# Optimization experiments

Measured on AMD Instinct MI355X. Metric: run time of the kernel, lower is better.

Reference implementation:

```python
import jax, jax.numpy as jnp
import numpy as np

DIM = 768
NUM_HEADS = 12
HEAD_DIM = DIM // NUM_HEADS
ORDER_H = 8
RENORM = True
B, N = 4, 1024


def setup_inputs() -> dict:
    key = jax.random.key(0)
    ks = jax.random.split(key, 8)
    return {
        "x": jax.random.normal(ks[0], (B, N, DIM), dtype=jnp.float32),
        "qkv_w": jax.random.normal(ks[1], (3 * DIM, DIM), dtype=jnp.float32) * (DIM ** -0.5),
        "qkv_b": jax.random.normal(ks[2], (3 * DIM,), dtype=jnp.float32) * 0.02,
        "proj_w": jax.random.normal(ks[3], (DIM, DIM), dtype=jnp.float32) * (DIM ** -0.5),
        "proj_b": jax.random.normal(ks[4], (DIM,), dtype=jnp.float32) * 0.02,
        "lamb": jax.random.normal(ks[5], (NUM_HEADS,), dtype=jnp.float32) * 0.1,
        "gamma": 1.0 + jax.random.normal(ks[6], (NUM_HEADS,), dtype=jnp.float32) * 0.1,
        "delta": jax.random.normal(ks[7], (NUM_HEADS,), dtype=jnp.float32) * 0.1,
    }


def reference(x, qkv_w, qkv_b, proj_w, proj_b, lamb, gamma, delta):
    Bx, Nx, C = x.shape
    scale = HEAD_DIM ** -0.5
    # qkv: [B,N,3C] -> [3,B,H,N,hd]
    qkv = (x @ qkv_w.T + qkv_b).reshape(Bx, Nx, 3, NUM_HEADS, HEAD_DIM)
    qkv = jnp.transpose(qkv, (2, 0, 3, 1, 4))
    q, k, v = qkv[0], qkv[1], qkv[2]
    attn = jax.nn.softmax(jnp.einsum("bhid,bhjd->bhij", q, k) * scale, axis=-1)
    I = jnp.eye(Nx, dtype=attn.dtype)
    # GFSA high-order term: (h-1)*(A - I)@A + A
    high = (ORDER_H - 1) * jnp.einsum("bhik,bhkj->bhij", attn - I, attn) + attn
    beta_ = lamb[None, :, None, None]
    gamma_ = gamma[None, :, None, None]
    delta_ = delta[None, :, None, None]
    attn = delta_ * I + gamma_ * attn + beta_ * high
    if RENORM:
        attn = jnp.maximum(attn, 0.0)
        attn = attn / (attn.sum(axis=-1, keepdims=True) + 1e-9)
    out = jnp.einsum("bhij,bhjd->bhid", attn, v)  # [B,H,N,hd]
    out = jnp.transpose(out, (0, 2, 1, 3)).reshape(Bx, Nx, C)
    return out @ proj_w.T + proj_b
```

## Files before the change

kernel.cpp:

```cpp
#include <hip/hip_runtime.h>
#include <hip/hip_bf16.h>

#define DIMC 768
#define NH 12
#define HD 64
#define BB 4
#define NN 1024
#define BHT 48
#define QKVC 2304

typedef unsigned short u16;
typedef __attribute__((ext_vector_type(4))) unsigned short u16x4;
typedef __attribute__((ext_vector_type(8))) unsigned short u16x8;
typedef __attribute__((ext_vector_type(8))) short s16x8;
typedef __attribute__((ext_vector_type(4))) float f32x4;

#define GLD16(g, l) __builtin_amdgcn_global_load_lds( \
    (__attribute__((address_space(1))) void*)(g),     \
    (__attribute__((address_space(3))) void*)(l), 16, 0, 0)

__device__ __forceinline__ u16 f2bf(float f) {
    unsigned u = __float_as_uint(f);
    return (u16)((u + 0x7FFF + ((u >> 16) & 1)) >> 16);
}
__device__ __forceinline__ float bf2f(u16 v) {
    return __uint_as_float(((unsigned)v) << 16);
}
struct bfp { u16 h, l; };
__device__ __forceinline__ bfp splitf(float f) {
    bfp r;
    r.h = f2bf(f);
    r.l = f2bf(f - bf2f(r.h));
    return r;
}

__device__ __forceinline__ int swz_linear() {
    const int nwg = gridDim.x * gridDim.y * gridDim.z;
    const int L = blockIdx.x + gridDim.x * (blockIdx.y + gridDim.y * blockIdx.z);
    return (L & 7) * (nwg >> 3) + (L >> 3);
}

__global__ __launch_bounds__(256) void split_f2b(
    const float* __restrict__ src, u16* __restrict__ hi, u16* __restrict__ lo,
    int n4)
{
    int idx = blockIdx.x * 256 + threadIdx.x;
    if (idx >= n4) return;
    float4 v = *(const float4*)&src[idx * 4];
    u16x4 h, l;
    bfp s;
    s = splitf(v.x); h[0] = s.h; l[0] = s.l;
    s = splitf(v.y); h[1] = s.h; l[1] = s.l;
    s = splitf(v.z); h[2] = s.h; l[2] = s.l;
    s = splitf(v.w); h[3] = s.h; l[3] = s.l;
    *(u16x4*)&hi[idx * 4] = h;
    *(u16x4*)&lo[idx * 4] = l;
}

__global__ __launch_bounds__(256, 3) void gemm3_mfma(
    int Mrows, int Nout, int K,
    const u16* __restrict__ Ahp, const u16* __restrict__ Alp,
    const u16* __restrict__ Bhp, const u16* __restrict__ Blp,
    const float* __restrict__ bias, float* __restrict__ C)
{
    __shared__ alignas(16) u16 sAh[128 * 32], sAl[128 * 32], sBh[128 * 32], sBl[128 * 32];
    const int tid = threadIdx.x;
    const int W = swz_linear();
    const int j0 = (W % gridDim.x) * 128, i0 = (W / gridDim.x) * 128;
    const int w = tid >> 6, l = tid & 63;
    const int wr = w >> 1, wc = w & 1;
    const int l15 = l & 15, kb4 = l >> 4;
    const int lrow = l >> 2, lch = (l & 3) * 8;

    f32x4 acc[4][4];
    const f32x4 zero = {0.f, 0.f, 0.f, 0.f};
#pragma unroll
    for (int a = 0; a < 4; ++a)
#pragma unroll
        for (int b = 0; b < 4; ++b) acc[a][b] = zero;

    for (int k0 = 0; k0 < K; k0 += 32) {
#pragma unroll
        for (int t = 0; t < 2; ++t) {
            const int r = w * 32 + t * 16;
            const size_t ar = (size_t)(i0 + r + lrow) * K + k0 + lch;
            const size_t br = (size_t)(j0 + r + lrow) * K + k0 + lch;
            GLD16(&Ahp[ar], &sAh[r * 32]);
            GLD16(&Alp[ar], &sAl[r * 32]);
            GLD16(&Bhp[br], &sBh[r * 32]);
            GLD16(&Blp[br], &sBl[r * 32]);
        }
        __syncthreads();

        s16x8 ah[4], al[4], bh[4], bl[4];
#pragma unroll
        for (int f = 0; f < 4; ++f) {
            const int ao = (wr * 64 + f * 16 + l15) * 32 + kb4 * 8;
            const int bo = (wc * 64 + f * 16 + l15) * 32 + kb4 * 8;
            ah[f] = *(const s16x8*)&sAh[ao];
            al[f] = *(const s16x8*)&sAl[ao];
            bh[f] = *(const s16x8*)&sBh[bo];
            bl[f] = *(const s16x8*)&sBl[bo];
        }
#pragma unroll
        for (int fr = 0; fr < 4; ++fr)
#pragma unroll
            for (int fc = 0; fc < 4; ++fc) {
                acc[fr][fc] = __builtin_amdgcn_mfma_f32_16x16x32_bf16(
                    ah[fr], bh[fc], acc[fr][fc], 0, 0, 0);
                acc[fr][fc] = __builtin_amdgcn_mfma_f32_16x16x32_bf16(
                    ah[fr], bl[fc], acc[fr][fc], 0, 0, 0);
                acc[fr][fc] = __builtin_amdgcn_mfma_f32_16x16x32_bf16(
                    al[fr], bh[fc], acc[fr][fc], 0, 0, 0);
            }
        __syncthreads();
    }

#pragma unroll
    for (int fr = 0; fr < 4; ++fr)
#pragma unroll
        for (int r = 0; r < 4; ++r) {
            const int gi = i0 + wr * 64 + fr * 16 + kb4 * 4 + r;
#pragma unroll
            for (int fc = 0; fc < 4; ++fc) {
                const int gj = j0 + wc * 64 + fc * 16 + l15;
                C[(size_t)gi * Nout + gj] = acc[fr][fc][r] + bias[gj];
            }
        }
}

__global__ __launch_bounds__(256, 3) void qkv_fused_mfma(
    const u16* __restrict__ Ahp, const u16* __restrict__ Alp,
    const u16* __restrict__ Bhp, const u16* __restrict__ Blp,
    const float* __restrict__ bias,
    u16* __restrict__ qh, u16* __restrict__ ql,
    u16* __restrict__ kh, u16* __restrict__ kl,
    u16* __restrict__ vth, u16* __restrict__ vtl)
{
    __shared__ alignas(16) u16 sAh[128 * 32], sAl[128 * 32], sBh[128 * 32], sBl[128 * 32];
    const int tid = threadIdx.x;
    const int W = swz_linear();
    const int j0 = (W % gridDim.x) * 128, i0 = (W / gridDim.x) * 128;
    const int w = tid >> 6, l = tid & 63;
    const int wr = w >> 1, wc = w & 1;
    const int l15 = l & 15, kb4 = l >> 4;
    const int lrow = l >> 2, lch = (l & 3) * 8;
    const int K = DIMC;

    f32x4 acc[4][4];
    const f32x4 zero = {0.f, 0.f, 0.f, 0.f};
#pragma unroll
    for (int a = 0; a < 4; ++a)
#pragma unroll
        for (int b = 0; b < 4; ++b) acc[a][b] = zero;

    for (int k0 = 0; k0 < K; k0 += 32) {
#pragma unroll
        for (int t = 0; t < 2; ++t) {
            const int r = w * 32 + t * 16;
            const size_t ar = (size_t)(i0 + r + lrow) * K + k0 + lch;
            const size_t br = (size_t)(j0 + r + lrow) * K + k0 + lch;
            GLD16(&Ahp[ar], &sAh[r * 32]);
            GLD16(&Alp[ar], &sAl[r * 32]);
            GLD16(&Bhp[br], &sBh[r * 32]);
            GLD16(&Blp[br], &sBl[r * 32]);
        }
        __syncthreads();

        s16x8 ah[4], al[4], bh[4], bl[4];
#pragma unroll
        for (int f = 0; f < 4; ++f) {
            const int ao = (wr * 64 + f * 16 + l15) * 32 + kb4 * 8;
            const int bo = (wc * 64 + f * 16 + l15) * 32 + kb4 * 8;
            ah[f] = *(const s16x8*)&sAh[ao];
            al[f] = *(const s16x8*)&sAl[ao];
            bh[f] = *(const s16x8*)&sBh[bo];
            bl[f] = *(const s16x8*)&sBl[bo];
        }
#pragma unroll
        for (int fr = 0; fr < 4; ++fr)
#pragma unroll
            for (int fc = 0; fc < 4; ++fc) {
                acc[fr][fc] = __builtin_amdgcn_mfma_f32_16x16x32_bf16(
                    ah[fr], bh[fc], acc[fr][fc], 0, 0, 0);
                acc[fr][fc] = __builtin_amdgcn_mfma_f32_16x16x32_bf16(
                    ah[fr], bl[fc], acc[fr][fc], 0, 0, 0);
                acc[fr][fc] = __builtin_amdgcn_mfma_f32_16x16x32_bf16(
                    al[fr], bh[fc], acc[fr][fc], 0, 0, 0);
            }
        __syncthreads();
    }

    const int part = j0 / DIMC;
    const int hbase = (j0 % DIMC) >> 6;
    const int h = hbase + wc;

#pragma unroll
    for (int fr = 0; fr < 4; ++fr) {
        const int rowbase = i0 + wr * 64 + fr * 16 + kb4 * 4;
        const int b = rowbase >> 10;
        const int n0 = rowbase & 1023;
        const int bh = b * NH + h;
#pragma unroll
        for (int fc = 0; fc < 4; ++fc) {
            const int gj = j0 + wc * 64 + fc * 16 + l15;
            const float bv = bias[gj];
            const int d = fc * 16 + l15;
            if (part == 0) {
#pragma unroll
                for (int r = 0; r < 4; ++r) {
                    bfp s = splitf((acc[fr][fc][r] + bv) * 0.125f);
                    const size_t o = ((size_t)bh * NN + n0 + r) * HD + d;
                    qh[o] = s.h; ql[o] = s.l;
                }
            } else if (part == 1) {
#pragma unroll
                for (int r = 0; r < 4; ++r) {
                    bfp s = splitf(acc[fr][fc][r] + bv);
                    const size_t o = ((size_t)bh * NN + n0 + r) * HD + d;
                    kh[o] = s.h; kl[o] = s.l;
                }
            } else {
                u16x4 hv, lv;
#pragma unroll
                for (int r = 0; r < 4; ++r) {
                    bfp s = splitf(acc[fr][fc][r] + bv);
                    hv[r] = s.h; lv[r] = s.l;
                }
                const size_t o = ((size_t)bh * HD + d) * NN + n0;
                *(u16x4*)&vth[o] = hv;
                *(u16x4*)&vtl[o] = lv;
            }
        }
    }
}

__global__ __launch_bounds__(256, 4) void qk_mfma(
    const u16* __restrict__ qh, const u16* __restrict__ ql,
    const u16* __restrict__ kh, const u16* __restrict__ kl,
    float* __restrict__ Sb, int h0)
{
    __shared__ alignas(16) u16 sAh[128 * 32], sAl[128 * 32], sBh[128 * 32], sBl[128 * 32];
    const int tid = threadIdx.x;
    const int W = swz_linear();
    const int bhl = W >> 6;
    const int ib = W & 63;
    const int j0 = (ib & 7) * 128, i0 = (ib >> 3) * 128;
    const int bh = h0 + bhl;
    const int w = tid >> 6, l = tid & 63;
    const int wr = w >> 1, wc = w & 1;
    const int l15 = l & 15, kb4 = l >> 4;
    const int lrow = l >> 2, lch = (l & 3) * 8;

    f32x4 acc[4][4];
    const f32x4 zero = {0.f, 0.f, 0.f, 0.f};
#pragma unroll
    for (int a = 0; a < 4; ++a)
#pragma unroll
        for (int b = 0; b < 4; ++b) acc[a][b] = zero;

    for (int k0 = 0; k0 < HD; k0 += 32) {
#pragma unroll
        for (int t = 0; t < 2; ++t) {
            const int r = w * 32 + t * 16;
            const size_t ar = ((size_t)bh * NN + i0 + r + lrow) * HD + k0 + lch;
            const size_t br = ((size_t)bh * NN + j0 + r + lrow) * HD + k0 + lch;
            GLD16(&qh[ar], &sAh[r * 32]);
            GLD16(&ql[ar], &sAl[r * 32]);
            GLD16(&kh[br], &sBh[r * 32]);
            GLD16(&kl[br], &sBl[r * 32]);
        }
        __syncthreads();

        s16x8 ah[4], al[4], bh[4], bl[4];
#pragma unroll
        for (int f = 0; f < 4; ++f) {
            const int ao = (wr * 64 + f * 16 + l15) * 32 + kb4 * 8;
            const int bo = (wc * 64 + f * 16 + l15) * 32 + kb4 * 8;
            ah[f] = *(const s16x8*)&sAh[ao];
            al[f] = *(const s16x8*)&sAl[ao];
            bh[f] = *(const s16x8*)&sBh[bo];
            bl[f] = *(const s16x8*)&sBl[bo];
        }
#pragma unroll
        for (int fr = 0; fr < 4; ++fr)
#pragma unroll
            for (int fc = 0; fc < 4; ++fc) {
                acc[fr][fc] = __builtin_amdgcn_mfma_f32_16x16x32_bf16(
                    ah[fr], bh[fc], acc[fr][fc], 0, 0, 0);
                acc[fr][fc] = __builtin_amdgcn_mfma_f32_16x16x32_bf16(
                    ah[fr], bl[fc], acc[fr][fc], 0, 0, 0);
                acc[fr][fc] = __builtin_amdgcn_mfma_f32_16x16x32_bf16(
                    al[fr], bh[fc], acc[fr][fc], 0, 0, 0);
            }
        __syncthreads();
    }

    float* Sh = Sb + (size_t)bhl * NN * NN;
#pragma unroll
    for (int fr = 0; fr < 4; ++fr)
#pragma unroll
        for (int r = 0; r < 4; ++r) {
            const int gi = i0 + wr * 64 + fr * 16 + kb4 * 4 + r;
#pragma unroll
            for (int fc = 0; fc < 4; ++fc) {
                const int gj = j0 + wc * 64 + fc * 16 + l15;
                Sh[(size_t)gi * NN + gj] = acc[fr][fc][r];
            }
        }
}

__global__ __launch_bounds__(256) void softmax_w(
    const float* __restrict__ Sb, u16* __restrict__ Abf)
{
    const int w = threadIdx.x >> 6, l = threadIdx.x & 63;
    const int row = blockIdx.x * 4 + w;
    const float* p = Sb + (size_t)row * NN;
    u16* q = Abf + (size_t)row * NN;

    float4 v[4];
    float m = -1e30f;
#pragma unroll
    for (int c = 0; c < 4; ++c) {
        v[c] = *(const float4*)&p[c * 256 + l * 4];
        m = fmaxf(m, fmaxf(fmaxf(v[c].x, v[c].y), fmaxf(v[c].z, v[c].w)));
    }
#pragma unroll
    for (int off = 32; off >= 1; off >>= 1) m = fmaxf(m, __shfl_xor(m, off));

    float s = 0.f;
#pragma unroll
    for (int c = 0; c < 4; ++c) {
        v[c].x = expf(v[c].x - m); v[c].y = expf(v[c].y - m);
        v[c].z = expf(v[c].z - m); v[c].w = expf(v[c].w - m);
        s += v[c].x + v[c].y + v[c].z + v[c].w;
    }
#pragma unroll
    for (int off = 32; off >= 1; off >>= 1) s += __shfl_xor(s, off);

    const float inv = 1.0f / s;
#pragma unroll
    for (int c = 0; c < 4; ++c) {
        u16x4 o;
        o[0] = f2bf(v[c].x * inv); o[1] = f2bf(v[c].y * inv);
        o[2] = f2bf(v[c].z * inv); o[3] = f2bf(v[c].w * inv);
        *(u16x4*)&q[c * 256 + l * 4] = o;
    }
}

__global__ __launch_bounds__(256, 4) void mpow_mfma(
    const u16* __restrict__ Abf, u16* __restrict__ Mb,
    const float* __restrict__ lamb, const float* __restrict__ gamma,
    const float* __restrict__ delta, int h0)
{
    __shared__ alignas(16) u16 sA[128 * 32], sB[128 * 32];
    const int tid = threadIdx.x;
    const int W = swz_linear();
    const int bz = W >> 6;
    const int ib = W & 63;
    const int j0 = (ib & 7) * 128, i0 = (ib >> 3) * 128;
    const int h = (h0 + bz) % NH;
    const u16* Ah = Abf + (size_t)bz * NN * NN;

    const int w = tid >> 6, l = tid & 63;
    const int wr = w >> 1, wc = w & 1;
    const int l15 = l & 15, kb4 = l >> 4;
    const int lrow = l >> 2;
    const int lchz = (((l & 3) ^ ((lrow >> 1) & 3)) * 8);
    const int swf = (l15 >> 1) & 3;
    const int kr = tid & 31;
    const int jc = (tid >> 5) * 16;
    const int krc = kr >> 3, kri = kr & 7;

    f32x4 acc[4][4];
    const f32x4 zero = {0.f, 0.f, 0.f, 0.f};
#pragma unroll
    for (int a = 0; a < 4; ++a)
#pragma unroll
        for (int b = 0; b < 4; ++b) acc[a][b] = zero;

    for (int k0 = 0; k0 < NN; k0 += 32) {
#pragma unroll
        for (int t = 0; t < 2; ++t) {
            const int r = w * 32 + t * 16;
            GLD16(&Ah[(size_t)(i0 + r + lrow) * NN + k0 + lchz], &sA[r * 32]);
        }
        {
            const u16* arow = &Ah[(size_t)(k0 + kr) * NN + j0 + jc];
            u16x8 b0 = *(const u16x8*)arow;
            u16x8 b1 = *(const u16x8*)(arow + 8);
#pragma unroll
            for (int e = 0; e < 8; ++e) {
                const int j1 = jc + e;
                const int j2 = jc + 8 + e;
                sB[j1 * 32 + ((krc ^ ((j1 >> 1) & 3)) * 8) + kri] = b0[e];
                sB[j2 * 32 + ((krc ^ ((j2 >> 1) & 3)) * 8) + kri] = b1[e];
            }
        }
        __syncthreads();

        s16x8 af[4], bf[4];
#pragma unroll
        for (int f = 0; f < 4; ++f) {
            const int co = (kb4 ^ swf) * 8;
            af[f] = *(const s16x8*)&sA[(wr * 64 + f * 16 + l15) * 32 + co];
            bf[f] = *(const s16x8*)&sB[(wc * 64 + f * 16 + l15) * 32 + co];
        }
#pragma unroll
        for (int fr = 0; fr < 4; ++fr)
#pragma unroll
            for (int fc = 0; fc < 4; ++fc)
                acc[fr][fc] = __builtin_amdgcn_mfma_f32_16x16x32_bf16(
                    af[fr], bf[fc], acc[fr][fc], 0, 0, 0);
        __syncthreads();
    }

    const float lam = lamb[h];
    const float c1 = gamma[h] - 6.0f * lam;
    const float c2 = 7.0f * lam;
    const float del = delta[h];
    u16* Mh = Mb + (size_t)bz * NN * NN;

#pragma unroll
    for (int fr = 0; fr < 4; ++fr)
#pragma unroll
        for (int r = 0; r < 4; ++r) {
            const int gi = i0 + wr * 64 + fr * 16 + kb4 * 4 + r;
#pragma unroll
            for (int fc = 0; fc < 4; ++fc) {
                const int gj = j0 + wc * 64 + fc * 16 + l15;
                const float a = bf2f(Ah[(size_t)gi * NN + gj]);
                float m = c2 * acc[fr][fc][r] + c1 * a + (gi == gj ? del : 0.f);
                m = fmaxf(m, 0.f);
                Mh[(size_t)gi * NN + gj] = f2bf(m);
            }
        }
}

__global__ __launch_bounds__(256, 4) void pv_mfma(
    const u16* __restrict__ Mb,
    const u16* __restrict__ vth, const u16* __restrict__ vtl,
    u16* __restrict__ aoh, u16* __restrict__ aol, int h0)
{
    __shared__ alignas(16) u16 sM[128 * 32], sVh[64 * 32], sVl[64 * 32];
    const int tid = threadIdx.x;
    const int W = swz_linear();
    const int bhl = W >> 3;
    const int i0 = (W & 7) * 128;
    const int bh = h0 + bhl;
    const int b = bh / NH, h = bh % NH;
    const u16* Mh = Mb + (size_t)bhl * NN * NN;
    const u16* vhb = vth + (size_t)bh * HD * NN;
    const u16* vlb = vtl + (size_t)bh * HD * NN;

    const int w = tid >> 6, l = tid & 63;
    const int l15 = l & 15, kb4 = l >> 4;
    const int lrow = l >> 2, lch = (l & 3) * 8;

    f32x4 acc[2][4], accs[2];
    const f32x4 zero = {0.f, 0.f, 0.f, 0.f};
#pragma unroll
    for (int a = 0; a < 2; ++a) {
#pragma unroll
        for (int c = 0; c < 4; ++c) acc[a][c] = zero;
        accs[a] = zero;
    }
    s16x8 ones;
#pragma unroll
    for (int e = 0; e < 8; ++e) ones[e] = (short)0x3F80;

    for (int k0 = 0; k0 < NN; k0 += 32) {
#pragma unroll
        for (int t = 0; t < 2; ++t) {
            const int r = w * 32 + t * 16;
            GLD16(&Mh[(size_t)(i0 + r + lrow) * NN + k0 + lch], &sM[r * 32]);
        }
        {
            const int r = w * 16;
            const size_t vr = (size_t)(r + lrow) * NN + k0 + lch;
            GLD16(&vhb[vr], &sVh[r * 32]);
            GLD16(&vlb[vr], &sVl[r * 32]);
        }
        __syncthreads();

        s16x8 af[2], bh[4], bl[4];
#pragma unroll
        for (int f = 0; f < 2; ++f)
            af[f] = *(const s16x8*)&sM[(w * 32 + f * 16 + l15) * 32 + kb4 * 8];
#pragma unroll
        for (int f = 0; f < 4; ++f) {
            bh[f] = *(const s16x8*)&sVh[(f * 16 + l15) * 32 + kb4 * 8];
            bl[f] = *(const s16x8*)&sVl[(f * 16 + l15) * 32 + kb4 * 8];
        }
#pragma unroll
        for (int fr = 0; fr < 2; ++fr) {
#pragma unroll
            for (int fc = 0; fc < 4; ++fc) {
                acc[fr][fc] = __builtin_amdgcn_mfma_f32_16x16x32_bf16(
                    af[fr], bh[fc], acc[fr][fc], 0, 0, 0);
                acc[fr][fc] = __builtin_amdgcn_mfma_f32_16x16x32_bf16(
                    af[fr], bl[fc], acc[fr][fc], 0, 0, 0);
            }
            accs[fr] = __builtin_amdgcn_mfma_f32_16x16x32_bf16(
                af[fr], ones, accs[fr], 0, 0, 0);
        }
        __syncthreads();
    }

#pragma unroll
    for (int fr = 0; fr < 2; ++fr)
#pragma unroll
        for (int r = 0; r < 4; ++r) {
            const int gi = i0 + w * 32 + fr * 16 + kb4 * 4 + r;
            const float inv = 1.0f / (accs[fr][r] + 1e-9f);
            const size_t ob = (size_t)(b * NN + gi) * DIMC + h * HD;
#pragma unroll
            for (int fc = 0; fc < 4; ++fc) {
                const int gd = fc * 16 + l15;
                bfp s = splitf(acc[fr][fc][r] * inv);
                aoh[ob + gd] = s.h;
                aol[ob + gd] = s.l;
            }
        }
}

extern "C" void kernel_launch(void* const* d_in, const int* in_sizes, int n_in,
                              void* d_out, int out_size, void* d_ws, size_t ws_size,
                              hipStream_t stream)
{
    const float* x      = (const float*)d_in[0];
    const float* qkv_w  = (const float*)d_in[1];
    const float* qkv_b  = (const float*)d_in[2];
    const float* proj_w = (const float*)d_in[3];
    const float* proj_b = (const float*)d_in[4];
    const float* lamb   = (const float*)d_in[5];
    const float* gamma  = (const float*)d_in[6];
    const float* delta  = (const float*)d_in[7];

    char* p = (char*)d_ws;
    u16* xh  = (u16*)p;                     p += (size_t)4096 * DIMC * 2;
    u16* xl  = (u16*)p;                     p += (size_t)4096 * DIMC * 2;
    u16* wh  = (u16*)p;                     p += (size_t)QKVC * DIMC * 2;
    u16* wl  = (u16*)p;                     p += (size_t)QKVC * DIMC * 2;
    u16* pwh = (u16*)p;                     p += (size_t)DIMC * DIMC * 2;
    u16* pwl = (u16*)p;                     p += (size_t)DIMC * DIMC * 2;
    u16* qh  = (u16*)p;                     p += (size_t)BHT * NN * HD * 2;
    u16* ql  = (u16*)p;                     p += (size_t)BHT * NN * HD * 2;
    u16* kh  = (u16*)p;                     p += (size_t)BHT * NN * HD * 2;
    u16* kl  = (u16*)p;                     p += (size_t)BHT * NN * HD * 2;
    u16* vth = (u16*)p;                     p += (size_t)BHT * HD * NN * 2;
    u16* vtl = (u16*)p;                     p += (size_t)BHT * HD * NN * 2;
    u16* aoh = (u16*)p;                     p += (size_t)4096 * DIMC * 2;
    u16* aol = (u16*)p;                     p += (size_t)4096 * DIMC * 2;
    const size_t fixed = (size_t)(p - (char*)d_ws);

    const size_t perh = (size_t)NN * NN * 4 + (size_t)NN * NN * 2;
    static const int choices[] = {48, 24, 16, 12, 8, 6, 4, 3, 2, 1};
    int CH = 1;
    for (int ci = 0; ci < 10; ++ci) {
        int c = choices[ci];
        if (fixed + (size_t)c * perh <= ws_size) { CH = c; break; }
    }

    float* Sb = (float*)p;                  p += (size_t)CH * NN * NN * 4;
    u16* Abf  = (u16*)p;                    p += (size_t)CH * NN * NN * 2;
    u16* Mb   = (u16*)Sb;

    split_f2b<<<dim3((4096 * DIMC / 4 + 255) / 256), 256, 0, stream>>>(x, xh, xl, 4096 * DIMC / 4);
    split_f2b<<<dim3((QKVC * DIMC / 4 + 255) / 256), 256, 0, stream>>>(qkv_w, wh, wl, QKVC * DIMC / 4);
    split_f2b<<<dim3((DIMC * DIMC / 4 + 255) / 256), 256, 0, stream>>>(proj_w, pwh, pwl, DIMC * DIMC / 4);

    qkv_fused_mfma<<<dim3(QKVC / 128, 4096 / 128), 256, 0, stream>>>(
        xh, xl, wh, wl, qkv_b, qh, ql, kh, kl, vth, vtl);

    for (int h0 = 0; h0 < BHT; h0 += CH) {
        qk_mfma<<<dim3(8, 8, CH), 256, 0, stream>>>(qh, ql, kh, kl, Sb, h0);
        softmax_w<<<dim3(CH * NN / 4), 256, 0, stream>>>(Sb, Abf);
        mpow_mfma<<<dim3(8, 8, CH), 256, 0, stream>>>(
            Abf, Mb, lamb, gamma, delta, h0);
        pv_mfma<<<dim3(8, CH), 256, 0, stream>>>(Mb, vth, vtl, aoh, aol, h0);
    }

    gemm3_mfma<<<dim3(DIMC / 128, 4096 / 128), 256, 0, stream>>>(
        4096, DIMC, DIMC, aoh, aol, pwh, pwl, proj_b, (float*)d_out);
}
```

Before: 417.8 us.

## Deepen mpow K tile to 64 and halve pv row tile for more blocks

The A@A kernel now stages 64-wide K slices per iteration, using a new 8-way XOR swizzle in LDS. That halves the number of barrier pairs and global-load rounds per output tile, at the cost of twice the LDS per block. Separately, the PV kernel shrinks its row tile from 128 to 64 and launches twice as many blocks, so more workgroups are spread over the CUs. The trade-off is that each V tile is reloaded by twice as many blocks.

```diff
diff --git a/kernel.cpp b/kernel.cpp
--- a/kernel.cpp
+++ b/kernel.cpp
@@ -353,7 +353,7 @@
     const float* __restrict__ lamb, const float* __restrict__ gamma,
     const float* __restrict__ delta, int h0)
 {
-    __shared__ alignas(16) u16 sA[128 * 32], sB[128 * 32];
+    __shared__ alignas(16) u16 sA[128 * 64], sB[128 * 64];
     const int tid = threadIdx.x;
     const int W = swz_linear();
     const int bz = W >> 6;
@@ -365,12 +365,10 @@
     const int w = tid >> 6, l = tid & 63;
     const int wr = w >> 1, wc = w & 1;
     const int l15 = l & 15, kb4 = l >> 4;
-    const int lrow = l >> 2;
-    const int lchz = (((l & 3) ^ ((lrow >> 1) & 3)) * 8);
-    const int swf = (l15 >> 1) & 3;
+    const int lr8 = l >> 3;
+    const int srck = ((l & 7) ^ lr8) * 8;
     const int kr = tid & 31;
     const int jc = (tid >> 5) * 16;
-    const int krc = kr >> 3, kri = kr & 7;
 
     f32x4 acc[4][4];
     const f32x4 zero = {0.f, 0.f, 0.f, 0.f};
@@ -379,39 +377,46 @@
 #pragma unroll
         for (int b = 0; b < 4; ++b) acc[a][b] = zero;
 
-    for (int k0 = 0; k0 < NN; k0 += 32) {
-#pragma unroll
-        for (int t = 0; t < 2; ++t) {
-            const int r = w * 32 + t * 16;
-            GLD16(&Ah[(size_t)(i0 + r + lrow) * NN + k0 + lchz], &sA[r * 32]);
-        }
-        {
-            const u16* arow = &Ah[(size_t)(k0 + kr) * NN + j0 + jc];
+    for (int k0 = 0; k0 < NN; k0 += 64) {
+#pragma unroll
+        for (int t = 0; t < 4; ++t) {
+            const int r = w * 32 + t * 8;
+            GLD16(&Ah[(size_t)(i0 + r + lr8) * NN + k0 + srck], &sA[r * 64]);
+        }
+#pragma unroll
+        for (int kk2 = 0; kk2 < 64; kk2 += 32) {
+            const int kloc = kk2 + kr;
+            const u16* arow = &Ah[(size_t)(k0 + kloc) * NN + j0 + jc];
             u16x8 b0 = *(const u16x8*)arow;
             u16x8 b1 = *(const u16x8*)(arow + 8);
+            const int kc = kloc >> 3, ke = kloc & 7;
 #pragma unroll
             for (int e = 0; e < 8; ++e) {
-                const int j1 = jc + e;
-                const int j2 = jc + 8 + e;
-                sB[j1 * 32 + ((krc ^ ((j1 >> 1) & 3)) * 8) + kri] = b0[e];
-                sB[j2 * 32 + ((krc ^ ((j2 >> 1) & 3)) * 8) + kri] = b1[e];
-            }
-        }
-        __syncthreads();
-
-        s16x8 af[4], bf[4];
-#pragma unroll
-        for (int f = 0; f < 4; ++f) {
-            const int co = (kb4 ^ swf) * 8;
-            af[f] = *(const s16x8*)&sA[(wr * 64 + f * 16 + l15) * 32 + co];
-            bf[f] = *(const s16x8*)&sB[(wc * 64 + f * 16 + l15) * 32 + co];
-        }
-#pragma unroll
-        for (int fr = 0; fr < 4; ++fr)
-#pragma unroll
-            for (int fc = 0; fc < 4; ++fc)
-                acc[fr][fc] = __builtin_amdgcn_mfma_f32_16x16x32_bf16(
-                    af[fr], bf[fc], acc[fr][fc], 0, 0, 0);
+                const int j1 = jc + e, j2 = jc + 8 + e;
+                sB[j1 * 64 + ((kc ^ (j1 & 7)) * 8) + ke] = b0[e];
+                sB[j2 * 64 + ((kc ^ (j2 & 7)) * 8) + ke] = b1[e];
+            }
+        }
+        __syncthreads();
+
+#pragma unroll
+        for (int kk = 0; kk < 64; kk += 32) {
+            const int ck = kk >> 3;
+            s16x8 af[4], bf[4];
+#pragma unroll
+            for (int f = 0; f < 4; ++f) {
+                const int ar_ = wr * 64 + f * 16 + l15;
+                const int br_ = wc * 64 + f * 16 + l15;
+                af[f] = *(const s16x8*)&sA[ar_ * 64 + (((ck + kb4) ^ (ar_ & 7)) * 8)];
+                bf[f] = *(const s16x8*)&sB[br_ * 64 + (((ck + kb4) ^ (br_ & 7)) * 8)];
+            }
+#pragma unroll
+            for (int fr = 0; fr < 4; ++fr)
+#pragma unroll
+                for (int fc = 0; fc < 4; ++fc)
+                    acc[fr][fc] = __builtin_amdgcn_mfma_f32_16x16x32_bf16(
+                        af[fr], bf[fc], acc[fr][fc], 0, 0, 0);
+        }
         __syncthreads();
     }
 
@@ -442,11 +447,11 @@
     const u16* __restrict__ vth, const u16* __restrict__ vtl,
     u16* __restrict__ aoh, u16* __restrict__ aol, int h0)
 {
-    __shared__ alignas(16) u16 sM[128 * 32], sVh[64 * 32], sVl[64 * 32];
+    __shared__ alignas(16) u16 sM[64 * 32], sVh[64 * 32], sVl[64 * 32];
     const int tid = threadIdx.x;
     const int W = swz_linear();
-    const int bhl = W >> 3;
-    const int i0 = (W & 7) * 128;
+    const int bhl = W >> 4;
+    const int i0 = (W & 15) * 64;
     const int bh = h0 + bhl;
     const int b = bh / NH, h = bh % NH;
     const u16* Mh = Mb + (size_t)bhl * NN * NN;
@@ -457,71 +462,56 @@
     const int l15 = l & 15, kb4 = l >> 4;
     const int lrow = l >> 2, lch = (l & 3) * 8;
 
-    f32x4 acc[2][4], accs[2];
+    f32x4 acc[4], accs;
     const f32x4 zero = {0.f, 0.f, 0.f, 0.f};
 #pragma unroll
-    for (int a = 0; a < 2; ++a) {
-#pragma unroll
-        for (int c = 0; c < 4; ++c) acc[a][c] = zero;
-        accs[a] = zero;
-    }
+    for (int c = 0; c < 4; ++c) acc[c] = zero;
+    accs = zero;
     s16x8 ones;
 #pragma unroll
     for (int e = 0; e < 8; ++e) ones[e] = (short)0x3F80;
 
     for (int k0 = 0; k0 < NN; k0 += 32) {
-#pragma unroll
-        for (int t = 0; t < 2; ++t) {
-            const int r = w * 32 + t * 16;
-            GLD16(&Mh[(size_t)(i0 + r + lrow) * NN + k0 + lch], &sM[r * 32]);
-        }
         {
             const int r = w * 16;
+            GLD16(&Mh[(size_t)(i0 + r + lrow) * NN + k0 + lch], &sM[r * 32]);
             const size_t vr = (size_t)(r + lrow) * NN + k0 + lch;
             GLD16(&vhb[vr], &sVh[r * 32]);
             GLD16(&vlb[vr], &sVl[r * 32]);
         }
         __syncthreads();
 
-        s16x8 af[2], bh[4], bl[4];
-#pragma unroll
-        for (int f = 0; f < 2; ++f)
-            af[f] = *(const s16x8*)&sM[(w * 32 + f * 16 + l15) * 32 + kb4 * 8];
+        s16x8 af, bh[4], bl[4];
+        af = *(const s16x8*)&sM[(w * 16 + l15) * 32 + kb4 * 8];
 #pragma unroll
         for (int f = 0; f < 4; ++f) {
             bh[f] = *(const s16x8*)&sVh[(f * 16 + l15) * 32 + kb4 * 8];
             bl[f] = *(const s16x8*)&sVl[(f * 16 + l15) * 32 + kb4 * 8];
         }
 #pragma unroll
-        for (int fr = 0; fr < 2; ++fr) {
-#pragma unroll
-            for (int fc = 0; fc < 4; ++fc) {
-                acc[fr][fc] = __builtin_amdgcn_mfma_f32_16x16x32_bf16(
-                    af[fr], bh[fc], acc[fr][fc], 0, 0, 0);
-                acc[fr][fc] = __builtin_amdgcn_mfma_f32_16x16x32_bf16(
-                    af[fr], bl[fc], acc[fr][fc], 0, 0, 0);
-            }
-            accs[fr] = __builtin_amdgcn_mfma_f32_16x16x32_bf16(
-                af[fr], ones, accs[fr], 0, 0, 0);
-        }
-        __syncthreads();
-    }
-
-#pragma unroll
-    for (int fr = 0; fr < 2; ++fr)
-#pragma unroll
-        for (int r = 0; r < 4; ++r) {
-            const int gi = i0 + w * 32 + fr * 16 + kb4 * 4 + r;
-            const float inv = 1.0f / (accs[fr][r] + 1e-9f);
-            const size_t ob = (size_t)(b * NN + gi) * DIMC + h * HD;
-#pragma unroll
-            for (int fc = 0; fc < 4; ++fc) {
-                const int gd = fc * 16 + l15;
-                bfp s = splitf(acc[fr][fc][r] * inv);
-                aoh[ob + gd] = s.h;
-                aol[ob + gd] = s.l;
-            }
-        }
+        for (int fc = 0; fc < 4; ++fc) {
+            acc[fc] = __builtin_amdgcn_mfma_f32_16x16x32_bf16(
+                af, bh[fc], acc[fc], 0, 0, 0);
+            acc[fc] = __builtin_amdgcn_mfma_f32_16x16x32_bf16(
+                af, bl[fc], acc[fc], 0, 0, 0);
+        }
+        accs = __builtin_amdgcn_mfma_f32_16x16x32_bf16(af, ones, accs, 0, 0, 0);
+        __syncthreads();
+    }
+
+#pragma unroll
+    for (int r = 0; r < 4; ++r) {
+        const int gi = i0 + w * 16 + kb4 * 4 + r;
+        const float inv = 1.0f / (accs[r] + 1e-9f);
+        const size_t ob = (size_t)(b * NN + gi) * DIMC + h * HD;
+#pragma unroll
+        for (int fc = 0; fc < 4; ++fc) {
+            const int gd = fc * 16 + l15;
+            bfp s = splitf(acc[fc][r] * inv);
+            aoh[ob + gd] = s.h;
+            aol[ob + gd] = s.l;
+        }
+    }
 }
 
 extern "C" void kernel_launch(void* const* d_in, const int* in_sizes, int n_in,
@@ -578,7 +568,7 @@
         softmax_w<<<dim3(CH * NN / 4), 256, 0, stream>>>(Sb, Abf);
         mpow_mfma<<<dim3(8, 8, CH), 256, 0, stream>>>(
             Abf, Mb, lamb, gamma, delta, h0);
-        pv_mfma<<<dim3(8, CH), 256, 0, stream>>>(Mb, vth, vtl, aoh, aol, h0);
+        pv_mfma<<<dim3(16, CH), 256, 0, stream>>>(Mb, vth, vtl, aoh, aol, h0);
     }
 
     gemm3_mfma<<<dim3(DIMC / 128, 4096 / 128), 256, 0, stream>>>(
```

New measurement: 401.4 us (median of 2 runs). 1.04x faster.
